# Performance work log

Measured on AMD Instinct MI355X. Metric: run time of the kernel, lower is better.

Reference implementation:

```python
import jax, jax.numpy as jnp
import numpy as np

N, K, C_IN, C_OUT, R = 100000, 256, 256, 256, 8


def setup_inputs() -> dict:
    key = jax.random.key(0)
    ks = jax.random.split(key, 8)
    return {
        "x": jax.random.normal(ks[0], (N, C_IN), dtype=jnp.float32),
        "eig_vals": 2.0 * jax.random.uniform(ks[1], (K,), dtype=jnp.float32),  # Laplacian eigvals in [0,2)
        "eig_vecs": jax.random.normal(ks[2], (N, K), dtype=jnp.float32) / np.sqrt(N),
        "h": jnp.asarray(0.5, dtype=jnp.float32),
        "alpha": jnp.asarray(0.1, dtype=jnp.float32),
        "c_0": jax.random.normal(ks[3], (C_OUT, C_IN), dtype=jnp.float32),
        "c_j_real": jax.random.normal(ks[4], (R, C_OUT, C_IN), dtype=jnp.float32),
        "c_j_imag": jax.random.normal(ks[5], (R, C_OUT, C_IN), dtype=jnp.float32),
    }


def reference(x, eig_vals, eig_vecs, h, alpha, c_0, c_j_real, c_j_imag):
    # Cayley transform per eigenvalue: base_k = (h*(lam_k - alpha) - i) / (h*(lam_k - alpha) + i)
    r = c_j_real.shape[0]
    c_j = c_j_real + 1j * c_j_imag                       # (r, out, in) complex64
    t = h * (eig_vals - alpha)                           # (K,)
    base = (t - 1j) / (t + 1j)                           # (K,) complex64, unit modulus
    # powers[j, k] = base_k ** (j+1), j = 0..r-1
    powers = base[None, :] ** jnp.arange(1, r + 1, dtype=jnp.float32)[:, None]  # (r, K)
    # per-eigenvalue real filter: c_0 + 2 * Re(sum_j c_j[j-1] * base^j)
    r_complex = jnp.einsum("rk,roi->koi", powers, c_j)   # (K, out, in)
    filters = c_0[None] + 2.0 * jnp.real(r_complex)      # (K, out, in)
    # res = sum_k v_k (v_k^T x) Q_k^T, batched across all eigenvalues
    P = eig_vecs.T @ x                                   # (K, in)
    Q = jnp.einsum("koi,ki->ko", filters, P)             # (K, out)
    return eig_vecs @ Q                                  # (N, out)
```

## Files before the change

kernel.cpp:

```cpp
#include <hip/hip_runtime.h>

#define NTOT 100000

typedef float f32x4 __attribute__((ext_vector_type(4)));
typedef float f32x2 __attribute__((ext_vector_type(2)));
typedef short s16x8 __attribute__((ext_vector_type(8)));
typedef short s16x4 __attribute__((ext_vector_type(4)));
typedef unsigned int u32x2 __attribute__((ext_vector_type(2)));
typedef unsigned short u16;
typedef unsigned int u32;

__device__ __forceinline__ u16 bfbits(float f) {
    return __builtin_bit_cast(u16, (__bf16)f);
}
__device__ __forceinline__ u32 packbf2(float a, float b) {
    return (u32)bfbits(a) | ((u32)bfbits(b) << 16);
}
__device__ __forceinline__ float bf2f(u16 u) {
    u32 v = ((u32)u) << 16;
    return __builtin_bit_cast(float, v);
}
__device__ __forceinline__ s16x8 cvt8(const float* __restrict__ p) {
    f32x4 lo = *(const f32x4*)p;
    f32x4 hi = *(const f32x4*)(p + 4);
    s16x8 r;
#pragma unroll
    for (int e = 0; e < 4; ++e) r[e] = (short)bfbits(lo[e]);
#pragma unroll
    for (int e = 0; e < 4; ++e) r[4 + e] = (short)bfbits(hi[e]);
    return r;
}

__device__ __forceinline__ s16x4 trread(unsigned a) {
    s16x4 d;
    asm volatile("ds_read_b64_tr_b16 %0, %1" : "=v"(d) : "v"(a));
    return d;
}
__device__ __forceinline__ s16x4 trread2k(unsigned a) {
    s16x4 d;
    asm volatile("ds_read_b64_tr_b16 %0, %1 offset:2048" : "=v"(d) : "v"(a));
    return d;
}
struct S2 { s16x4 lo, hi; };
__device__ __forceinline__ s16x8 cat44(s16x4 lo, s16x4 hi) {
    S2 s{lo, hi};
    return __builtin_bit_cast(s16x8, s);
}
#define LGKM0_FENCE()                                         \
    do {                                                      \
        asm volatile("s_waitcnt lgkmcnt(0)" ::: "memory");    \
        __builtin_amdgcn_sched_barrier(0);                    \
    } while (0)

__global__ void k_weights(const float* __restrict__ ev, const float* __restrict__ hp,
                          const float* __restrict__ ap, float* __restrict__ br,
                          float* __restrict__ bi) {
    int k = threadIdx.x;
    float h = hp[0], alpha = ap[0];
    float t = h * (ev[k] - alpha);
    float inv = 1.0f / (t * t + 1.0f);
    float b_re = (t * t - 1.0f) * inv;
    float b_im = -2.0f * t * inv;
    float cr = b_re, ci = b_im;
    br[k] = cr; bi[k] = ci;
#pragma unroll
    for (int j = 1; j < 8; ++j) {
        float nr = cr * b_re - ci * b_im;
        float ni = cr * b_im + ci * b_re;
        cr = nr; ci = ni;
        br[j * 256 + k] = cr;
        bi[j * 256 + k] = ci;
    }
}

__global__ __launch_bounds__(1024, 4) void k_gemm1(
    const float* __restrict__ E, const float* __restrict__ X,
    u16* __restrict__ Pp, int NB) {
    __shared__ alignas(16) u16 Et[2][8192];
    __shared__ alignas(16) u16 Xt[2][8192];

    int chunk = blockIdx.x;
    int nStart = chunk * NB;
    int nEnd = min(nStart + NB, NTOT);
    if (nEnd <= nStart) return;

    int t = threadIdx.x, lane = t & 63, w = t >> 6;
    int wk = w & 3, wi = w >> 2;
    int l15 = lane & 15, lhi = lane >> 4;
    int rg = w >> 1, qh = w & 1;

    unsigned EtB = (unsigned)(size_t)&Et[0][0];
    unsigned XtB = (unsigned)(size_t)&Xt[0][0];

    int q0 = qh * 2, q1 = q0 + 1;
    int d0 = ((lane & 3) + q0) & 3, d1 = ((lane & 3) + q1) & 3;
    int g0 = q0 * 16 + (lane >> 2), g1 = q1 * 16 + (lane >> 2);
    unsigned wb0 = (unsigned)((rg * 16 + (g0 >> 2)) * 128 + d0 * 32 + (g0 & 3) * 8);
    unsigned wb1 = (unsigned)((rg * 16 + (g1 >> 2)) * 128 + d1 * 32 + (g1 & 3) * 8);
    unsigned aB = EtB + (unsigned)(lhi * 4096 + wk * 512 + l15 * 8);
    unsigned bB = XtB + (unsigned)(lhi * 4096 + wi * 512 + l15 * 8);

    f32x4 vE0, vE1, vX0, vX1;
    f32x4 acc[4][4] = {};
    int nwin = (nEnd - nStart + 31) >> 5;

#define G1_LOAD(WIN)                                                        \
    {                                                                       \
        int nb_ = nStart + (WIN) * 32 + rg * 4;                             \
        int r0_ = nb_ + d0, r1_ = nb_ + d1;                                 \
        int a0_ = (r0_ < nEnd) ? r0_ : nStart;                              \
        int a1_ = (r1_ < nEnd) ? r1_ : nStart;                              \
        float m0_ = (r0_ < nEnd) ? 1.f : 0.f;                               \
        float m1_ = (r1_ < nEnd) ? 1.f : 0.f;                               \
        vE0 = *(const f32x4*)(E + (size_t)a0_ * 256 + g0 * 4) * m0_;        \
        vE1 = *(const f32x4*)(E + (size_t)a1_ * 256 + g1 * 4) * m1_;        \
        vX0 = *(const f32x4*)(X + (size_t)a0_ * 256 + g0 * 4) * m0_;        \
        vX1 = *(const f32x4*)(X + (size_t)a1_ * 256 + g1 * 4) * m1_;        \
    }

#define G1_WRITE(BUF)                                                       \
    {                                                                       \
        unsigned bo_ = (unsigned)(BUF) * 16384u;                            \
        *(u32x2*)((char*)Et + bo_ + wb0) =                                  \
            (u32x2){packbf2(vE0[0], vE0[1]), packbf2(vE0[2], vE0[3])};      \
        *(u32x2*)((char*)Et + bo_ + wb1) =                                  \
            (u32x2){packbf2(vE1[0], vE1[1]), packbf2(vE1[2], vE1[3])};      \
        *(u32x2*)((char*)Xt + bo_ + wb0) =                                  \
            (u32x2){packbf2(vX0[0], vX0[1]), packbf2(vX0[2], vX0[3])};      \
        *(u32x2*)((char*)Xt + bo_ + wb1) =                                  \
            (u32x2){packbf2(vX1[0], vX1[1]), packbf2(vX1[2], vX1[3])};      \
    }

#define G1_COMPUTE(BUF)                                                     \
    {                                                                       \
        unsigned bo_ = (unsigned)(BUF) * 16384u;                            \
        unsigned aB_ = aB + bo_, bB_ = bB + bo_;                            \
        s16x4 ta0[4], ta1[4], tb0[4], tb1[4];                               \
        _Pragma("unroll") for (int m = 0; m < 4; ++m) {                     \
            ta0[m] = trread(aB_ + m * 128);                                 \
            ta1[m] = trread2k(aB_ + m * 128);                               \
        }                                                                   \
        _Pragma("unroll") for (int c = 0; c < 4; ++c) {                     \
            tb0[c] = trread(bB_ + c * 128);                                 \
            tb1[c] = trread2k(bB_ + c * 128);                               \
        }                                                                   \
        LGKM0_FENCE();                                                      \
        s16x8 a[4], b[4];                                                   \
        _Pragma("unroll") for (int m = 0; m < 4; ++m) a[m] = cat44(ta0[m], ta1[m]); \
        _Pragma("unroll") for (int c = 0; c < 4; ++c) b[c] = cat44(tb0[c], tb1[c]); \
        _Pragma("unroll") for (int m = 0; m < 4; ++m)                       \
            _Pragma("unroll") for (int c = 0; c < 4; ++c)                   \
                acc[m][c] = __builtin_amdgcn_mfma_f32_16x16x32_bf16(        \
                    a[m], b[c], acc[m][c], 0, 0, 0);                        \
    }

    G1_LOAD(0);
    G1_WRITE(0);
    G1_LOAD(1);
    asm volatile("s_waitcnt lgkmcnt(0)" ::: "memory");
    __builtin_amdgcn_s_barrier();
    for (int win = 0; win < nwin; ++win) {
        int cur = win & 1;
        G1_COMPUTE(cur);
        if (win + 1 < nwin) G1_WRITE(cur ^ 1);
        if (win + 2 < nwin) G1_LOAD(win + 2);
        asm volatile("s_waitcnt lgkmcnt(0)" ::: "memory");
        __builtin_amdgcn_s_barrier();
    }
#undef G1_LOAD
#undef G1_WRITE
#undef G1_COMPUTE

    u16* dst = Pp + (size_t)chunk * 65536;
#pragma unroll
    for (int m = 0; m < 4; ++m) {
#pragma unroll
        for (int cf = 0; cf < 4; ++cf) {
            int ii = wi * 64 + cf * 16 + l15;
#pragma unroll
            for (int r = 0; r < 4; ++r) {
                int kk = wk * 64 + m * 16 + lhi * 4 + r;
                dst[kk * 256 + ii] = bfbits(acc[m][cf][r]);
            }
        }
    }
}

__global__ void k_reduceA(const u32* __restrict__ Pp32,
                          f32x2* __restrict__ Pf, int cpg) {
    int g = blockIdx.x >> 7;
    int idx = (blockIdx.x & 127) * 256 + threadIdx.x;
    int c0 = g * cpg;
    float s0 = 0.f, s1 = 0.f;
    for (int c = c0; c < c0 + cpg; ++c) {
        u32 vv = Pp32[(size_t)c * 32768 + idx];
        s0 += bf2f((u16)(vv & 0xffff));
        s1 += bf2f((u16)(vv >> 16));
    }
    Pf[(size_t)g * 32768 + idx] = (f32x2){s0, s1};
}

__global__ void k_reduceB(const f32x2* __restrict__ Pf,
                          u32* __restrict__ Pb32, int G) {
    int idx = blockIdx.x * 256 + threadIdx.x;
    float s0 = 0.f, s1 = 0.f;
    for (int g = 0; g < G; ++g) {
        f32x2 v = Pf[(size_t)g * 32768 + idx];
        s0 += v[0]; s1 += v[1];
    }
    Pb32[idx] = packbf2(s0, s1);
}

__global__ __launch_bounds__(256, 4) void k_smallgemm(
    const u16* __restrict__ Pb, const float* __restrict__ c0,
    const float* __restrict__ cjr, const float* __restrict__ cji,
    float* __restrict__ T) {
    int c = blockIdx.x >> 3;
    int k0 = (blockIdx.x & 7) * 32;
    const float* W = (c == 0) ? c0 : (c <= 8 ? (cjr + (size_t)(c - 1) * 65536)
                                             : (cji + (size_t)(c - 9) * 65536));
    int t = threadIdx.x, lane = t & 63, wi = t >> 6;
    int l15 = lane & 15, lhi = lane >> 4;
    f32x4 acc[2][4] = {};
    for (int is = 0; is < 256; is += 32) {
        s16x8 a[2], b[4];
#pragma unroll
        for (int m = 0; m < 2; ++m)
            a[m] = *(const s16x8*)(Pb + (k0 + m * 16 + l15) * 256 + is + lhi * 8);
#pragma unroll
        for (int cf = 0; cf < 4; ++cf)
            b[cf] = cvt8(W + (size_t)(wi * 64 + cf * 16 + l15) * 256 + is + lhi * 8);
#pragma unroll
        for (int m = 0; m < 2; ++m)
#pragma unroll
            for (int cf = 0; cf < 4; ++cf)
                acc[m][cf] = __builtin_amdgcn_mfma_f32_16x16x32_bf16(
                    a[m], b[cf], acc[m][cf], 0, 0, 0);
    }
    float* dst = T + (size_t)c * 65536;
#pragma unroll
    for (int m = 0; m < 2; ++m) {
#pragma unroll
        for (int cf = 0; cf < 4; ++cf) {
            int oo = wi * 64 + cf * 16 + l15;
#pragma unroll
            for (int r = 0; r < 4; ++r) {
                int kk = k0 + m * 16 + lhi * 4 + r;
                dst[kk * 256 + oo] = acc[m][cf][r];
            }
        }
    }
}

__global__ void k_combine(const float* __restrict__ T, const float* __restrict__ br,
                          const float* __restrict__ bi, u16* __restrict__ Qt) {
    int t = threadIdx.x;
    int k = blockIdx.x * 4 + (t >> 6);
    int o4 = (t & 63) * 4;
    f32x4 q = *(const f32x4*)(T + (size_t)k * 256 + o4);
#pragma unroll
    for (int j = 0; j < 8; ++j) {
        float brv = br[j * 256 + k], biv = bi[j * 256 + k];
        f32x4 tr = *(const f32x4*)(T + (size_t)(1 + j) * 65536 + k * 256 + o4);
        f32x4 ti = *(const f32x4*)(T + (size_t)(9 + j) * 65536 + k * 256 + o4);
        q += 2.0f * (brv * tr - biv * ti);
    }
#pragma unroll
    for (int e = 0; e < 4; ++e) Qt[(size_t)(o4 + e) * 256 + k] = bfbits(q[e]);
}

__global__ __launch_bounds__(512, 4) void k_gemm2(
    const float* __restrict__ E, const u16* __restrict__ Qt,
    float* __restrict__ out) {
    __shared__ alignas(16) u16 Ebuf[2][32 * 256];

    int b0 = blockIdx.x;
    int b = (b0 & 7) * 64 + (b0 >> 3);
    int og = b & 1;
    int slab = b >> 1;
    int tile0 = slab * 12 + min(slab, 53);
    int nt = (slab < 53) ? 13 : 12;

    int t = threadIdx.x, lane = t & 63, w = t >> 6;
    int l15 = lane & 15, lhi = lane >> 4;
    int wn = w & 1, wo = w >> 1;
    int obase = og * 128 + wo * 32;
    int nrow = wn * 16 + l15;

    s16x8 af[2][8];
#pragma unroll
    for (int m = 0; m < 2; ++m)
#pragma unroll
        for (int ks = 0; ks < 8; ++ks)
            af[m][ks] = *(const s16x8*)(Qt + (size_t)(obase + m * 16 + l15) * 256 +
                                        ks * 32 + lhi * 8);

    f32x4 rvA[4], rvB[4];

#define G2_LOADE(TI, RV)                                                    \
    {                                                                       \
        int nb0_ = (tile0 + (TI)) * 32 + w * 4;                             \
        _Pragma("unroll") for (int j = 0; j < 4; ++j)                       \
            RV[j] = *(const f32x4*)(E + (size_t)(nb0_ + j) * 256 + lane * 4); \
    }

#define G2_WRITEE(RV, BUF)                                                  \
    _Pragma("unroll") for (int j = 0; j < 4; ++j) {                         \
        int r_ = w * 4 + j;                                                 \
        *(u32x2*)((char*)Ebuf[BUF] + r_ * 512 +                             \
                  (((lane >> 1) ^ (r_ & 7)) * 16) + (lane & 1) * 8) =       \
            (u32x2){packbf2(RV[j][0], RV[j][1]), packbf2(RV[j][2], RV[j][3])}; \
    }

#define G2_TILE(I, BUF, WRV, LRV)                                           \
    {                                                                       \
        f32x4 acc[2] = {};                                                  \
        const char* Eb_ = (const char*)Ebuf[BUF];                           \
        _Pragma("unroll") for (int ks = 0; ks < 8; ++ks) {                  \
            s16x8 ef = *(const s16x8*)(Eb_ + nrow * 512 +                   \
                        (((ks * 4 + lhi) ^ (nrow & 7)) * 16));              \
            _Pragma("unroll") for (int m = 0; m < 2; ++m)                   \
                acc[m] = __builtin_amdgcn_mfma_f32_16x16x32_bf16(           \
                    af[m][ks], ef, acc[m], 0, 0, 0);                        \
        }                                                                   \
        int n_ = (tile0 + (I)) * 32 + wn * 16 + l15;                        \
        _Pragma("unroll") for (int m = 0; m < 2; ++m)                       \
            *(f32x4*)(out + (size_t)n_ * 256 + obase + m * 16 + lhi * 4) =  \
                acc[m];                                                     \
        if ((I) + 1 < nt) G2_WRITEE(WRV, (BUF) ^ 1);                        \
        if ((I) + 2 < nt) G2_LOADE((I) + 2, LRV);                           \
        asm volatile("s_waitcnt lgkmcnt(0)" ::: "memory");                  \
        __builtin_amdgcn_s_barrier();                                       \
    }

    G2_LOADE(0, rvA);
    G2_WRITEE(rvA, 0);
    G2_LOADE(1, rvB);
    asm volatile("s_waitcnt lgkmcnt(0)" ::: "memory");
    __builtin_amdgcn_s_barrier();

    for (int i = 0; i < nt; i += 2) {
        G2_TILE(i, 0, rvB, rvA);
        if (i + 1 < nt)
            G2_TILE(i + 1, 1, rvA, rvB);
    }
#undef G2_LOADE
#undef G2_WRITEE
#undef G2_TILE
}

extern "C" void kernel_launch(void* const* d_in, const int* in_sizes, int n_in,
                              void* d_out, int out_size, void* d_ws, size_t ws_size,
                              hipStream_t stream) {
    const float* x   = (const float*)d_in[0];
    const float* ev  = (const float*)d_in[1];
    const float* E   = (const float*)d_in[2];
    const float* hp  = (const float*)d_in[3];
    const float* ap  = (const float*)d_in[4];
    const float* c0  = (const float*)d_in[5];
    const float* cjr = (const float*)d_in[6];
    const float* cji = (const float*)d_in[7];
    float* out = (float*)d_out;

    char* ws = (char*)d_ws;
    float* br = (float*)(ws + 0);
    float* bi = (float*)(ws + 8192);
    u16*   Pb = (u16*)(ws + 16384);
    u16*   Qt = (u16*)(ws + 147456);
    float* T  = (float*)(ws + 278528);

    u16* Pp = (u16*)d_out;
    f32x2* Pf = (f32x2*)((char*)d_out + 33554432);
    const int chunks = 256;
    const int NB = 391;
    const int G = 16, CPG = 16;

    k_weights<<<1, 256, 0, stream>>>(ev, hp, ap, br, bi);
    k_gemm1<<<chunks, 1024, 0, stream>>>(E, x, Pp, NB);
    k_reduceA<<<G * 128, 256, 0, stream>>>((const u32*)Pp, Pf, CPG);
    k_reduceB<<<128, 256, 0, stream>>>(Pf, (u32*)Pb, G);
    k_smallgemm<<<17 * 8, 256, 0, stream>>>(Pb, c0, cjr, cji, T);
    k_combine<<<64, 256, 0, stream>>>(T, br, bi, Qt);
    k_gemm2<<<512, 512, 0, stream>>>(E, Qt, out);
}
```

Baseline: 135.8 us.

## Split gemm1 across K halves into 512-thread blocks and fold weights into combine

```diff
diff --git a/kernel.cpp b/kernel.cpp
--- a/kernel.cpp
+++ b/kernel.cpp
@@ -36,6 +36,11 @@
     asm volatile("ds_read_b64_tr_b16 %0, %1" : "=v"(d) : "v"(a));
     return d;
 }
+__device__ __forceinline__ s16x4 trread1k(unsigned a) {
+    s16x4 d;
+    asm volatile("ds_read_b64_tr_b16 %0, %1 offset:1024" : "=v"(d) : "v"(a));
+    return d;
+}
 __device__ __forceinline__ s16x4 trread2k(unsigned a) {
     s16x4 d;
     asm volatile("ds_read_b64_tr_b16 %0, %1 offset:2048" : "=v"(d) : "v"(a));
@@ -52,93 +57,80 @@
         __builtin_amdgcn_sched_barrier(0);                    \
     } while (0)
 
-__global__ void k_weights(const float* __restrict__ ev, const float* __restrict__ hp,
-                          const float* __restrict__ ap, float* __restrict__ br,
-                          float* __restrict__ bi) {
-    int k = threadIdx.x;
-    float h = hp[0], alpha = ap[0];
-    float t = h * (ev[k] - alpha);
-    float inv = 1.0f / (t * t + 1.0f);
-    float b_re = (t * t - 1.0f) * inv;
-    float b_im = -2.0f * t * inv;
-    float cr = b_re, ci = b_im;
-    br[k] = cr; bi[k] = ci;
-#pragma unroll
-    for (int j = 1; j < 8; ++j) {
-        float nr = cr * b_re - ci * b_im;
-        float ni = cr * b_im + ci * b_re;
-        cr = nr; ci = ni;
-        br[j * 256 + k] = cr;
-        bi[j * 256 + k] = ci;
-    }
-}
-
-__global__ __launch_bounds__(1024, 4) void k_gemm1(
+__global__ __launch_bounds__(512, 4) void k_gemm1(
     const float* __restrict__ E, const float* __restrict__ X,
     u16* __restrict__ Pp, int NB) {
-    __shared__ alignas(16) u16 Et[2][8192];
+    __shared__ alignas(16) u16 Et[2][4096];
     __shared__ alignas(16) u16 Xt[2][8192];
 
-    int chunk = blockIdx.x;
+    int bx = blockIdx.x;
+    int chunk = bx >> 1, kh = bx & 1, k0 = kh * 128;
     int nStart = chunk * NB;
     int nEnd = min(nStart + NB, NTOT);
     if (nEnd <= nStart) return;
 
     int t = threadIdx.x, lane = t & 63, w = t >> 6;
-    int wk = w & 3, wi = w >> 2;
+    int wk = w & 1, wi = w >> 1;
     int l15 = lane & 15, lhi = lane >> 4;
-    int rg = w >> 1, qh = w & 1;
+    int lq = lane >> 2, ld = lane & 3;
 
     unsigned EtB = (unsigned)(size_t)&Et[0][0];
     unsigned XtB = (unsigned)(size_t)&Xt[0][0];
 
-    int q0 = qh * 2, q1 = q0 + 1;
-    int d0 = ((lane & 3) + q0) & 3, d1 = ((lane & 3) + q1) & 3;
-    int g0 = q0 * 16 + (lane >> 2), g1 = q1 * 16 + (lane >> 2);
-    unsigned wb0 = (unsigned)((rg * 16 + (g0 >> 2)) * 128 + d0 * 32 + (g0 & 3) * 8);
-    unsigned wb1 = (unsigned)((rg * 16 + (g1 >> 2)) * 128 + d1 * 32 + (g1 & 3) * 8);
-    unsigned aB = EtB + (unsigned)(lhi * 4096 + wk * 512 + l15 * 8);
+    unsigned aB = EtB + (unsigned)(lhi * 2048 + wk * 512 + l15 * 8);
     unsigned bB = XtB + (unsigned)(lhi * 4096 + wi * 512 + l15 * 8);
 
-    f32x4 vE0, vE1, vX0, vX1;
+    f32x4 vE[2], vX[4];
     f32x4 acc[4][4] = {};
     int nwin = (nEnd - nStart + 31) >> 5;
 
 #define G1_LOAD(WIN)                                                        \
     {                                                                       \
-        int nb_ = nStart + (WIN) * 32 + rg * 4;                             \
-        int r0_ = nb_ + d0, r1_ = nb_ + d1;                                 \
-        int a0_ = (r0_ < nEnd) ? r0_ : nStart;                              \
-        int a1_ = (r1_ < nEnd) ? r1_ : nStart;                              \
-        float m0_ = (r0_ < nEnd) ? 1.f : 0.f;                               \
-        float m1_ = (r1_ < nEnd) ? 1.f : 0.f;                               \
-        vE0 = *(const f32x4*)(E + (size_t)a0_ * 256 + g0 * 4) * m0_;        \
-        vE1 = *(const f32x4*)(E + (size_t)a1_ * 256 + g1 * 4) * m1_;        \
-        vX0 = *(const f32x4*)(X + (size_t)a0_ * 256 + g0 * 4) * m0_;        \
-        vX1 = *(const f32x4*)(X + (size_t)a1_ * 256 + g1 * 4) * m1_;        \
+        int n0_ = nStart + (WIN) * 32 + w * 4;                              \
+        _Pragma("unroll") for (int qe = 0; qe < 2; ++qe) {                  \
+            int r_ = n0_ + ((ld + qe) & 3);                                 \
+            int a_ = (r_ < nEnd) ? r_ : nStart;                             \
+            float m_ = (r_ < nEnd) ? 1.f : 0.f;                             \
+            vE[qe] = *(const f32x4*)(E + (size_t)a_ * 256 + k0 +            \
+                                     (qe * 16 + lq) * 4) * m_;              \
+        }                                                                   \
+        _Pragma("unroll") for (int q = 0; q < 4; ++q) {                     \
+            int r_ = n0_ + ((ld + q) & 3);                                  \
+            int a_ = (r_ < nEnd) ? r_ : nStart;                             \
+            float m_ = (r_ < nEnd) ? 1.f : 0.f;                             \
+            vX[q] = *(const f32x4*)(X + (size_t)a_ * 256 +                  \
+                                    (q * 16 + lq) * 4) * m_;                \
+        }                                                                   \
     }
 
 #define G1_WRITE(BUF)                                                       \
     {                                                                       \
-        unsigned bo_ = (unsigned)(BUF) * 16384u;                            \
-        *(u32x2*)((char*)Et + bo_ + wb0) =                                  \
-            (u32x2){packbf2(vE0[0], vE0[1]), packbf2(vE0[2], vE0[3])};      \
-        *(u32x2*)((char*)Et + bo_ + wb1) =                                  \
-            (u32x2){packbf2(vE1[0], vE1[1]), packbf2(vE1[2], vE1[3])};      \
-        *(u32x2*)((char*)Xt + bo_ + wb0) =                                  \
-            (u32x2){packbf2(vX0[0], vX0[1]), packbf2(vX0[2], vX0[3])};      \
-        *(u32x2*)((char*)Xt + bo_ + wb1) =                                  \
-            (u32x2){packbf2(vX1[0], vX1[1]), packbf2(vX1[2], vX1[3])};      \
+        _Pragma("unroll") for (int qe = 0; qe < 2; ++qe) {                  \
+            int g_ = qe * 16 + lq, d_ = (ld + qe) & 3;                      \
+            unsigned by_ = (unsigned)(BUF) * 8192u +                        \
+                (unsigned)((w * 8 + (g_ >> 2)) * 128 + d_ * 32 + (g_ & 3) * 8); \
+            *(u32x2*)((char*)Et + by_) =                                    \
+                (u32x2){packbf2(vE[qe][0], vE[qe][1]),                      \
+                        packbf2(vE[qe][2], vE[qe][3])};                     \
+        }                                                                   \
+        _Pragma("unroll") for (int q = 0; q < 4; ++q) {                     \
+            int g_ = q * 16 + lq, d_ = (ld + q) & 3;                        \
+            unsigned by_ = (unsigned)(BUF) * 16384u +                       \
+                (unsigned)((w * 16 + (g_ >> 2)) * 128 + d_ * 32 + (g_ & 3) * 8); \
+            *(u32x2*)((char*)Xt + by_) =                                    \
+                (u32x2){packbf2(vX[q][0], vX[q][1]),                        \
+                        packbf2(vX[q][2], vX[q][3])};                       \
+        }                                                                   \
     }
 
 #define G1_COMPUTE(BUF)                                                     \
     {                                                                       \
-        unsigned bo_ = (unsigned)(BUF) * 16384u;                            \
-        unsigned aB_ = aB + bo_, bB_ = bB + bo_;                            \
+        unsigned aB_ = aB + (unsigned)(BUF) * 8192u;                        \
+        unsigned bB_ = bB + (unsigned)(BUF) * 16384u;                       \
         s16x4 ta0[4], ta1[4], tb0[4], tb1[4];                               \
         _Pragma("unroll") for (int m = 0; m < 4; ++m) {                     \
             ta0[m] = trread(aB_ + m * 128);                                 \
-            ta1[m] = trread2k(aB_ + m * 128);                               \
+            ta1[m] = trread1k(aB_ + m * 128);                               \
         }                                                                   \
         _Pragma("unroll") for (int c = 0; c < 4; ++c) {                     \
             tb0[c] = trread(bB_ + c * 128);                                 \
@@ -179,7 +171,7 @@
             int ii = wi * 64 + cf * 16 + l15;
 #pragma unroll
             for (int r = 0; r < 4; ++r) {
-                int kk = wk * 64 + m * 16 + lhi * 4 + r;
+                int kk = k0 + wk * 64 + m * 16 + lhi * 4 + r;
                 dst[kk * 256 + ii] = bfbits(acc[m][cf][r]);
             }
         }
@@ -252,18 +244,27 @@
     }
 }
 
-__global__ void k_combine(const float* __restrict__ T, const float* __restrict__ br,
-                          const float* __restrict__ bi, u16* __restrict__ Qt) {
+__global__ void k_combine(const float* __restrict__ T, const float* __restrict__ ev,
+                          const float* __restrict__ hp, const float* __restrict__ ap,
+                          u16* __restrict__ Qt) {
     int t = threadIdx.x;
     int k = blockIdx.x * 4 + (t >> 6);
     int o4 = (t & 63) * 4;
+    float h = hp[0], alpha = ap[0];
+    float tt = h * (ev[k] - alpha);
+    float inv = 1.0f / (tt * tt + 1.0f);
+    float bre = (tt * tt - 1.0f) * inv;
+    float bim = -2.0f * tt * inv;
+    float cr = bre, ci = bim;
     f32x4 q = *(const f32x4*)(T + (size_t)k * 256 + o4);
 #pragma unroll
     for (int j = 0; j < 8; ++j) {
-        float brv = br[j * 256 + k], biv = bi[j * 256 + k];
         f32x4 tr = *(const f32x4*)(T + (size_t)(1 + j) * 65536 + k * 256 + o4);
         f32x4 ti = *(const f32x4*)(T + (size_t)(9 + j) * 65536 + k * 256 + o4);
-        q += 2.0f * (brv * tr - biv * ti);
+        q += 2.0f * (cr * tr - ci * ti);
+        float nr = cr * bre - ci * bim;
+        float ni = cr * bim + ci * bre;
+        cr = nr; ci = ni;
     }
 #pragma unroll
     for (int e = 0; e < 4; ++e) Qt[(size_t)(o4 + e) * 256 + k] = bfbits(q[e]);
@@ -363,8 +364,6 @@
     float* out = (float*)d_out;
 
     char* ws = (char*)d_ws;
-    float* br = (float*)(ws + 0);
-    float* bi = (float*)(ws + 8192);
     u16*   Pb = (u16*)(ws + 16384);
     u16*   Qt = (u16*)(ws + 147456);
     float* T  = (float*)(ws + 278528);
@@ -375,11 +374,10 @@
     const int NB = 391;
     const int G = 16, CPG = 16;
 
-    k_weights<<<1, 256, 0, stream>>>(ev, hp, ap, br, bi);
-    k_gemm1<<<chunks, 1024, 0, stream>>>(E, x, Pp, NB);
+    k_gemm1<<<2 * chunks, 512, 0, stream>>>(E, x, Pp, NB);
     k_reduceA<<<G * 128, 256, 0, stream>>>((const u32*)Pp, Pf, CPG);
     k_reduceB<<<128, 256, 0, stream>>>(Pf, (u32*)Pb, G);
     k_smallgemm<<<17 * 8, 256, 0, stream>>>(Pb, c0, cjr, cji, T);
-    k_combine<<<64, 256, 0, stream>>>(T, br, bi, Qt);
+    k_combine<<<64, 256, 0, stream>>>(T, ev, hp, ap, Qt);
     k_gemm2<<<512, 512, 0, stream>>>(E, Qt, out);
 }
```

Result: slower. 172.6 us (+27.1%).
